# Kernel tuning notes

Hardware: AMD Instinct MI355X
Metric: run time of the kernel (lower is better)

The kernel has to match this reference:

```python
import jax, jax.numpy as jnp
import numpy as np

N_INST = 8      # number of instance labels present in target (== len(torch.unique(gt)))
DELTA_V = 0.5
ALPHA = 1.0
CLAMP_MAX = 100000.0


def setup_inputs() -> dict:
    key = jax.random.key(0)
    k1, k2 = jax.random.split(key)
    prediction = jax.random.normal(k1, (4, 16, 512, 512), dtype=jnp.float32)
    target = jax.random.randint(k2, (4, 512, 512), 0, N_INST)  # all labels 0..7 present whp
    return {"prediction": prediction, "target": target}


def _loss(prediction, target):
    B, nf, H, W = prediction.shape
    N = H * W
    pred = prediction.reshape(B, nf, N)                    # [B, nf, N]
    gt = target.reshape(B, N)                              # [B, N]
    # one-hot instance masks (unique sorted labels == arange(N_INST) by construction)
    mask = (gt[:, :, None] == jnp.arange(N_INST)[None, None, :]).astype(pred.dtype)  # [B, N, C]
    counts = mask.sum(axis=1)                              # [B, C] pixels per instance
    # per-instance means: sum of masked embeddings / counts
    means = jnp.einsum('bfn,bnc->bfc', pred, mask) / counts[:, None, :]  # [B, nf, C]
    # mu_expand - pred_masked = mask * (mu - pred); norm over feature dim
    diff = (means[:, :, None, :] - pred[:, :, :, None]) * mask[:, None, :, :]  # [B, nf, N, C]
    sq = jnp.sum(diff * diff, axis=1)                      # [B, N, C]
    # safe sqrt (zero where diff==0, matching torch.norm subgradient)
    d = jnp.where(sq > 0, jnp.sqrt(jnp.where(sq > 0, sq, 1.0)), 0.0)
    dist = jnp.clip(d - DELTA_V, 0.0, CLAMP_MAX) ** 2      # [B, N, C]
    # faithful to source: torch.sum(distance) is a full scalar reduce, then / counts, sum, / C
    l_var = dist.sum(axis=(1, 2)) * (1.0 / counts).sum(axis=1) / N_INST  # [B]
    return ALPHA * jnp.sum(l_var)


def reference(prediction, target):
    return _loss(prediction, target)
```

## Files before the change

kernel.cpp:

```cpp
#include <hip/hip_runtime.h>

#define NF   16
#define C    8
#define NB   4
#define NPIX (512*512)

#define CH      16
#define CPX     (NPIX / CH)
#define SITERS  (CPX / (256 * 4))

#define DG      256
#define DCHUNK  (NPIX / DG)

#define WS_PSUM 0
#define WS_PCNT (NB * NF * CH * 8)
#define WS_MEAN (WS_PCNT + NB * CH * 8)
#define WS_INV  (WS_MEAN + NB * 128)
#define WS_POUT (WS_INV + NB)

__global__ __launch_bounds__(256) void sums_kernel(const float* __restrict__ pred,
                                                   const int* __restrict__ tgt,
                                                   float* __restrict__ ws) {
    const int t    = threadIdx.x;
    const int lane = t & 63;
    const int wave = t >> 6;
    const int ch   = blockIdx.x;
    const int f    = blockIdx.y;
    const int b    = blockIdx.z;

    const float* pf = pred + ((size_t)b * NF + f) * NPIX + ch * CPX;
    const int*   tg = tgt  + (size_t)b * NPIX + ch * CPX;

    float acc[8];
#pragma unroll
    for (int c = 0; c < 8; ++c) acc[c] = 0.0f;
    float cnt[8];
#pragma unroll
    for (int c = 0; c < 8; ++c) cnt[c] = 0.0f;

    for (int it = 0; it < SITERS; ++it) {
        const int px = it * 1024 + t * 4;
        int4   lab = *(const int4*)(tg + px);
        float4 p   = *(const float4*)(pf + px);
        float m0[8], m1[8], m2[8], m3[8];
#pragma unroll
        for (int c = 0; c < 8; ++c) {
            m0[c] = (lab.x == c) ? 1.0f : 0.0f;
            m1[c] = (lab.y == c) ? 1.0f : 0.0f;
            m2[c] = (lab.z == c) ? 1.0f : 0.0f;
            m3[c] = (lab.w == c) ? 1.0f : 0.0f;
        }
#pragma unroll
        for (int c = 0; c < 8; ++c)
            acc[c] += m0[c] * p.x + m1[c] * p.y + m2[c] * p.z + m3[c] * p.w;
        if (f == 0) {
#pragma unroll
            for (int c = 0; c < 8; ++c)
                cnt[c] += m0[c] + m1[c] + m2[c] + m3[c];
        }
    }

#pragma unroll
    for (int off = 32; off > 0; off >>= 1)
#pragma unroll
        for (int c = 0; c < 8; ++c)
            acc[c] += __shfl_xor(acc[c], off);
    if (f == 0) {
#pragma unroll
        for (int off = 32; off > 0; off >>= 1)
#pragma unroll
            for (int c = 0; c < 8; ++c)
                cnt[c] += __shfl_xor(cnt[c], off);
    }

    __shared__ float sred[4][8];
    __shared__ float scred[4][8];
    if (lane == 0) {
#pragma unroll
        for (int c = 0; c < 8; ++c) sred[wave][c] = acc[c];
        if (f == 0)
#pragma unroll
            for (int c = 0; c < 8; ++c) scred[wave][c] = cnt[c];
    }
    __syncthreads();
    if (t < 8)
        ws[WS_PSUM + (((size_t)b * NF + f) * CH + ch) * 8 + t] =
            sred[0][t] + sred[1][t] + sred[2][t] + sred[3][t];
    if (f == 0 && t >= 8 && t < 16) {
        const int c = t - 8;
        ws[WS_PCNT + (b * CH + ch) * 8 + c] =
            scred[0][c] + scred[1][c] + scred[2][c] + scred[3][c];
    }
}

__global__ void means_kernel(float* __restrict__ ws) {
    __shared__ float scnt[32];
    const int t = threadIdx.x;
    if (t < 32) {
        const int b = t >> 3, c = t & 7;
        float s = 0.0f;
#pragma unroll
        for (int ch = 0; ch < CH; ++ch)
            s += ws[WS_PCNT + (b * CH + ch) * 8 + c];
        scnt[t] = s;
    }
    __syncthreads();
    const int b = t >> 7, fc = t & 127, f = fc >> 3, c = fc & 7;
    float s = 0.0f;
#pragma unroll
    for (int ch = 0; ch < CH; ++ch)
        s += ws[WS_PSUM + (((size_t)b * NF + f) * CH + ch) * 8 + c];
    ws[WS_MEAN + b * 128 + fc] = s / scnt[b * 8 + c];
    if (fc == 0) {
        float iv = 0.0f;
#pragma unroll
        for (int c8 = 0; c8 < 8; ++c8) iv += 1.0f / scnt[b * 8 + c8];
        ws[WS_INV + b] = iv;
    }
}

__global__ __launch_bounds__(256) void dist_kernel(const float* __restrict__ pred,
                                                   const int* __restrict__ tgt,
                                                   const float* __restrict__ ws,
                                                   float* __restrict__ pout) {
    __shared__ float s_means[C * NF];
    __shared__ float s_red[4];
    const int tid = threadIdx.x;
    const int b   = blockIdx.y;
    if (tid < C * NF) s_means[tid] = ws[WS_MEAN + b * 128 + tid];
    const float invs = ws[WS_INV + b];
    __syncthreads();

    const float* predb = pred + (size_t)b * NF * NPIX;
    const int*   tgtb  = tgt  + (size_t)b * NPIX;

    const int base = blockIdx.x * DCHUNK + tid * 4;
    int4 lab = *(const int4*)(tgtb + base);
    float s0 = 0.f, s1 = 0.f, s2 = 0.f, s3 = 0.f;
#pragma unroll
    for (int f = 0; f < NF; ++f) {
        float4 p = *(const float4*)(predb + f * NPIX + base);
        float d0 = s_means[f * C + lab.x] - p.x;
        float d1 = s_means[f * C + lab.y] - p.y;
        float d2 = s_means[f * C + lab.z] - p.z;
        float d3 = s_means[f * C + lab.w] - p.w;
        s0 += d0 * d0; s1 += d1 * d1; s2 += d2 * d2; s3 += d3 * d3;
    }
    float t0 = fminf(fmaxf(sqrtf(s0) - 0.5f, 0.0f), 100000.0f);
    float t1 = fminf(fmaxf(sqrtf(s1) - 0.5f, 0.0f), 100000.0f);
    float t2 = fminf(fmaxf(sqrtf(s2) - 0.5f, 0.0f), 100000.0f);
    float t3 = fminf(fmaxf(sqrtf(s3) - 0.5f, 0.0f), 100000.0f);
    float acc = t0 * t0 + t1 * t1 + t2 * t2 + t3 * t3;

#pragma unroll
    for (int off = 32; off > 0; off >>= 1) acc += __shfl_down(acc, off);
    const int lane = tid & 63, wave = tid >> 6;
    if (lane == 0) s_red[wave] = acc;
    __syncthreads();
    if (tid == 0) {
        float tot = s_red[0] + s_red[1] + s_red[2] + s_red[3];
        pout[b * DG + blockIdx.x] = tot * invs * 0.125f;
    }
}

__global__ void final_kernel(const float* __restrict__ pout, float* __restrict__ out) {
    __shared__ float sr[8];
    const int t = threadIdx.x;
    float v = pout[t] + pout[t + 512];
#pragma unroll
    for (int off = 32; off > 0; off >>= 1) v += __shfl_xor(v, off);
    if ((t & 63) == 0) sr[t >> 6] = v;
    __syncthreads();
    if (t == 0) {
        float s = 0.0f;
#pragma unroll
        for (int i = 0; i < 8; ++i) s += sr[i];
        out[0] = s;
    }
}

extern "C" void kernel_launch(void* const* d_in, const int* in_sizes, int n_in,
                              void* d_out, int out_size, void* d_ws, size_t ws_size,
                              hipStream_t stream) {
    const float* pred = (const float*)d_in[0];
    const int*   tgt  = (const int*)d_in[1];
    float* out = (float*)d_out;
    float* ws  = (float*)d_ws;

    sums_kernel<<<dim3(CH, NF, NB), dim3(256), 0, stream>>>(pred, tgt, ws);
    means_kernel<<<dim3(1), dim3(512), 0, stream>>>(ws);
    dist_kernel<<<dim3(DG, NB), dim3(256), 0, stream>>>(pred, tgt, ws, ws + WS_POUT);
    final_kernel<<<dim3(1), dim3(512), 0, stream>>>(ws + WS_POUT, out);
}
```

Measured before the change: 119.0 us.

## Fold means reduction into dist kernel and widen sums grid

Removes the single-block means kernel launch. Each dist block now reduces the per-chunk partial sums and counts itself to build means and the inverse-count sum in shared memory. The sums kernel uses four times as many pixel chunks, giving more blocks and better occupancy, and its inner loop is fully unrolled. The cost is that every dist block redundantly reads about 64 partials per mean/count value from the workspace before it starts, which adds latency at the head of each block.

```diff
diff --git a/kernel.cpp b/kernel.cpp
--- a/kernel.cpp
+++ b/kernel.cpp
@@ -5,7 +5,7 @@
 #define NB   4
 #define NPIX (512*512)
 
-#define CH      16
+#define CH      64
 #define CPX     (NPIX / CH)
 #define SITERS  (CPX / (256 * 4))
 
@@ -14,9 +14,7 @@
 
 #define WS_PSUM 0
 #define WS_PCNT (NB * NF * CH * 8)
-#define WS_MEAN (WS_PCNT + NB * CH * 8)
-#define WS_INV  (WS_MEAN + NB * 128)
-#define WS_POUT (WS_INV + NB)
+#define WS_POUT (WS_PCNT + NB * CH * 8)
 
 __global__ __launch_bounds__(256) void sums_kernel(const float* __restrict__ pred,
                                                    const int* __restrict__ tgt,
@@ -38,6 +36,7 @@
 #pragma unroll
     for (int c = 0; c < 8; ++c) cnt[c] = 0.0f;
 
+#pragma unroll
     for (int it = 0; it < SITERS; ++it) {
         const int px = it * 1024 + t * 4;
         int4   lab = *(const int4*)(tg + px);
@@ -93,42 +92,52 @@
     }
 }
 
-__global__ void means_kernel(float* __restrict__ ws) {
-    __shared__ float scnt[32];
-    const int t = threadIdx.x;
-    if (t < 32) {
-        const int b = t >> 3, c = t & 7;
-        float s = 0.0f;
-#pragma unroll
-        for (int ch = 0; ch < CH; ++ch)
-            s += ws[WS_PCNT + (b * CH + ch) * 8 + c];
-        scnt[t] = s;
-    }
-    __syncthreads();
-    const int b = t >> 7, fc = t & 127, f = fc >> 3, c = fc & 7;
-    float s = 0.0f;
-#pragma unroll
-    for (int ch = 0; ch < CH; ++ch)
-        s += ws[WS_PSUM + (((size_t)b * NF + f) * CH + ch) * 8 + c];
-    ws[WS_MEAN + b * 128 + fc] = s / scnt[b * 8 + c];
-    if (fc == 0) {
-        float iv = 0.0f;
-#pragma unroll
-        for (int c8 = 0; c8 < 8; ++c8) iv += 1.0f / scnt[b * 8 + c8];
-        ws[WS_INV + b] = iv;
-    }
-}
-
 __global__ __launch_bounds__(256) void dist_kernel(const float* __restrict__ pred,
                                                    const int* __restrict__ tgt,
                                                    const float* __restrict__ ws,
                                                    float* __restrict__ pout) {
-    __shared__ float s_means[C * NF];
+    __shared__ float sm_p[2][128];
+    __shared__ float scnt_p[8][8];
+    __shared__ float scnt[8];
+    __shared__ float s_means[128];
+    __shared__ float s_invs;
     __shared__ float s_red[4];
     const int tid = threadIdx.x;
     const int b   = blockIdx.y;
-    if (tid < C * NF) s_means[tid] = ws[WS_MEAN + b * 128 + tid];
-    const float invs = ws[WS_INV + b];
+
+    if (tid < 64) {
+        const int c = tid & 7, grp = tid >> 3;
+        float s = 0.0f;
+#pragma unroll
+        for (int i = 0; i < 8; ++i)
+            s += ws[WS_PCNT + (b * CH + grp * 8 + i) * 8 + c];
+        scnt_p[grp][c] = s;
+    }
+    {
+        const int fc = tid & 127, half = tid >> 7;
+        const int f = fc >> 3, c = fc & 7;
+        float s = 0.0f;
+#pragma unroll
+        for (int i = 0; i < 32; ++i)
+            s += ws[WS_PSUM + (((size_t)b * NF + f) * CH + half * 32 + i) * 8 + c];
+        sm_p[half][fc] = s;
+    }
+    __syncthreads();
+    if (tid < 8) {
+        float s = 0.0f;
+#pragma unroll
+        for (int grp = 0; grp < 8; ++grp) s += scnt_p[grp][tid];
+        scnt[tid] = s;
+    }
+    __syncthreads();
+    if (tid < 128)
+        s_means[tid] = (sm_p[0][tid] + sm_p[1][tid]) / scnt[tid & 7];
+    if (tid == 0) {
+        float iv = 0.0f;
+#pragma unroll
+        for (int c = 0; c < 8; ++c) iv += 1.0f / scnt[c];
+        s_invs = iv;
+    }
     __syncthreads();
 
     const float* predb = pred + (size_t)b * NF * NPIX;
@@ -159,7 +168,7 @@
     __syncthreads();
     if (tid == 0) {
         float tot = s_red[0] + s_red[1] + s_red[2] + s_red[3];
-        pout[b * DG + blockIdx.x] = tot * invs * 0.125f;
+        pout[b * DG + blockIdx.x] = tot * s_invs * 0.125f;
     }
 }
 
@@ -188,7 +197,6 @@
     float* ws  = (float*)d_ws;
 
     sums_kernel<<<dim3(CH, NF, NB), dim3(256), 0, stream>>>(pred, tgt, ws);
-    means_kernel<<<dim3(1), dim3(512), 0, stream>>>(ws);
     dist_kernel<<<dim3(DG, NB), dim3(256), 0, stream>>>(pred, tgt, ws, ws + WS_POUT);
     final_kernel<<<dim3(1), dim3(512), 0, stream>>>(ws + WS_POUT, out);
 }
```

Result: no change. 118.7 us (-0.3%).
